# Kernel optimization log

Measured on AMD Instinct MI355X. Metric: run time of the kernel, lower is better.

## Reference

```python
import jax, jax.numpy as jnp
import numpy as np

TEMPERATURE = 0.5
W_WITHIN = 1.0
W_CROSS = 0.5
MARGIN = 0.1


def setup_inputs() -> dict:
    key = jax.random.key(0)
    k1, k2 = jax.random.split(key)
    features = jax.random.normal(k1, (8192, 256), dtype=jnp.float32)
    gene_labels = jax.random.randint(k2, (8192,), 0, 200, dtype=jnp.int64 if jax.config.jax_enable_x64 else jnp.int32)
    return {"features": features, "gene_labels": gene_labels}


def reference(features, gene_labels):
    B = features.shape[0]
    # L2-normalize rows, full pairwise cosine similarity / temperature
    fn = features / jnp.linalg.norm(features, axis=1, keepdims=True)
    sim = (fn @ fn.T) / TEMPERATURE  # [B, B]

    same = gene_labels[:, None] == gene_labels[None, :]  # [B, B]
    eye = jnp.eye(B, dtype=bool)
    same_off = same & ~eye            # same-gene, off-diagonal (gene_similarity)
    neg = ~same                       # different-gene pairs (cross_gene_mask)
    has_neg = neg.any(axis=1)

    # Per-anchor logsumexp over negatives (sim of anchor i to all different-gene samples)
    neg_sim = jnp.where(neg, sim, -jnp.inf)
    lse_neg = jax.scipy.special.logsumexp(neg_sim, axis=1)
    lse_neg = jnp.where(has_neg, lse_neg, 0.0)  # rows with no negatives are masked out below

    # Within-gene loss: for each unordered same-gene pair (i<j) with gene != -1 and
    # anchor i having >=1 negative: CE([sim_ij, neg_sims_i], label=0)
    #   = -sim_ij + logaddexp(sim_ij, lse_neg_i) = softplus(lse_neg_i - sim_ij)
    upper = jnp.triu(jnp.ones((B, B), dtype=bool), k=1)
    valid_gene = (gene_labels != -1)[:, None]
    pair_mask = same_off & upper & valid_gene & has_neg[:, None]
    within_gene_loss = jnp.where(pair_mask, jax.nn.softplus(lse_neg[:, None] - sim), 0.0).sum()

    # Cross-gene loss: mean over all ordered different-gene pairs of relu(sim - margin)
    cross_cnt = neg.sum()
    cross_sum = jnp.where(neg, jax.nn.relu(sim - MARGIN), 0.0).sum()
    cross_gene_loss = jnp.where(cross_cnt > 0, cross_sum / jnp.maximum(cross_cnt, 1).astype(sim.dtype), 0.0)

    total_loss = W_WITHIN * within_gene_loss + W_CROSS * cross_gene_loss
    num_within_gene_pairs = same_off.sum().astype(sim.dtype)
    num_cross_gene_pairs = cross_cnt
    return total_loss, within_gene_loss, cross_gene_loss, num_within_gene_pairs, num_cross_gene_pairs
```

## Files before the change

kernel.cpp:

```cpp
#include <hip/hip_runtime.h>
#include <math.h>

#define B_N   8192
#define D_K   256
#define NGENE 200
#define MAXN  512

typedef short  bf16x8 __attribute__((ext_vector_type(8)));
typedef float  f32x4  __attribute__((ext_vector_type(4)));

#define OFF_FNBF    0u
#define OFF_LPART   4194304u
#define OFF_HIST    4718592u
#define OFF_OFFS    4719616u
#define OFF_SORTED  4720640u
#define OFF_CROSSP  4753408u
#define OFF_WITHINP 4755456u
#define OFF_CCORR   4756480u

__device__ __forceinline__ unsigned short f2bf(float f) {
    unsigned int u = __float_as_uint(f);
    unsigned int r = u + 0x7fffu + ((u >> 16) & 1u);
    return (unsigned short)(r >> 16);
}
__device__ __forceinline__ float bf2f_lo(unsigned int u) { return __uint_as_float(u << 16); }
__device__ __forceinline__ float bf2f_hi(unsigned int u) { return __uint_as_float(u & 0xffff0000u); }

__global__ __launch_bounds__(256) void k_np(const float* __restrict__ feat,
                                            const int* __restrict__ lab,
                                            unsigned short* __restrict__ fnbf,
                                            int* __restrict__ hist,
                                            int* __restrict__ offs,
                                            int* __restrict__ sorted) {
    if (blockIdx.x < 2048) {
        int wave = threadIdx.x >> 6, lane = threadIdx.x & 63;
        int row  = blockIdx.x * 4 + wave;
        const float4* src = reinterpret_cast<const float4*>(feat + (size_t)row * D_K);
        float4 v = src[lane];
        float ss = v.x * v.x + v.y * v.y + v.z * v.z + v.w * v.w;
#pragma unroll
        for (int m = 1; m < 64; m <<= 1) ss += __shfl_xor(ss, m);
        float rn = 1.0f / sqrtf(ss);
        ushort4 o;
        o.x = f2bf(v.x * rn); o.y = f2bf(v.y * rn);
        o.z = f2bf(v.z * rn); o.w = f2bf(v.w * rn);
        reinterpret_cast<ushort4*>(fnbf + (size_t)row * D_K)[lane] = o;
        return;
    }
    __shared__ int sh_hist[256], sh_scan[256], sh_cur[256];
    int t = threadIdx.x;
    sh_hist[t] = 0;
    __syncthreads();
    for (int i = t; i < B_N; i += 256) {
        int lb = lab[i];
        if (lb >= 0 && lb < NGENE) atomicAdd(&sh_hist[lb], 1);
    }
    __syncthreads();
    int v = sh_hist[t];
    sh_scan[t] = v;
    __syncthreads();
#pragma unroll
    for (int d = 1; d < 256; d <<= 1) {
        int x = (t >= d) ? sh_scan[t - d] : 0;
        __syncthreads();
        sh_scan[t] += x;
        __syncthreads();
    }
    int excl = sh_scan[t] - v;
    sh_cur[t] = excl;
    if (t < NGENE) { hist[t] = v; offs[t] = excl; }
    __syncthreads();
    for (int i = t; i < B_N; i += 256) {
        int lb = lab[i];
        if (lb >= 0 && lb < NGENE) {
            int pos = atomicAdd(&sh_cur[lb], 1);
            sorted[pos] = i;
        }
    }
}

#define GLOAD8(arr, vo) do {                                                                   \
    asm volatile("global_load_dwordx4 %0, %1, %2 offset:0"   : "=v"(arr[0]) : "v"(vo), "s"(fb)); \
    asm volatile("global_load_dwordx4 %0, %1, %2 offset:64"  : "=v"(arr[1]) : "v"(vo), "s"(fb)); \
    asm volatile("global_load_dwordx4 %0, %1, %2 offset:128" : "=v"(arr[2]) : "v"(vo), "s"(fb)); \
    asm volatile("global_load_dwordx4 %0, %1, %2 offset:192" : "=v"(arr[3]) : "v"(vo), "s"(fb)); \
    asm volatile("global_load_dwordx4 %0, %1, %2 offset:256" : "=v"(arr[4]) : "v"(vo), "s"(fb)); \
    asm volatile("global_load_dwordx4 %0, %1, %2 offset:320" : "=v"(arr[5]) : "v"(vo), "s"(fb)); \
    asm volatile("global_load_dwordx4 %0, %1, %2 offset:384" : "=v"(arr[6]) : "v"(vo), "s"(fb)); \
    asm volatile("global_load_dwordx4 %0, %1, %2 offset:448" : "=v"(arr[7]) : "v"(vo), "s"(fb)); \
} while (0)

#define GL_LDS16(gp, lp)                                                          \
    __builtin_amdgcn_global_load_lds(                                             \
        (const __attribute__((address_space(1))) unsigned int*)(gp),              \
        (__attribute__((address_space(3))) unsigned int*)(lp), 16, 0, 0)

#define Z4 ((f32x4){0.f, 0.f, 0.f, 0.f})
#define MFMA(A, B, C) __builtin_amdgcn_mfma_f32_16x16x32_bf16(A, B, C, 0, 0, 0)

#define EPI(AC, LS, CS) do {                                    \
    _Pragma("unroll")                                           \
    for (int r = 0; r < 4; ++r) {                               \
        float av = AC[r];                                       \
        LS[r] += __expf(2.0f * av);                             \
        CS += fmaxf(av - 0.05f, 0.f);                           \
    }                                                           \
} while (0)

#define WAIT_VM(n) do { asm volatile("s_waitcnt vmcnt(" #n ")" ::: "memory"); \
                        __builtin_amdgcn_sched_barrier(0); } while (0)

#define WAIT_LGKM0 do { asm volatile("s_waitcnt lgkmcnt(0)" ::: "memory"); \
                        __builtin_amdgcn_sched_barrier(0); } while (0)

#define STAGE_W(BOFF, T) do {                                                      \
    const char* gt = gw + (unsigned)(T) * 8192u;                                   \
    _Pragma("unroll")                                                              \
    for (int q = 0; q < 8; ++q)                                                    \
        GL_LDS16(gt + sv[q], smem_c + wbase + (BOFF) + q * 1024u);                 \
} while (0)

__global__ __launch_bounds__(256, 2) void k_pairwise(const unsigned short* __restrict__ fnbf,
                                                     float* __restrict__ l_part,
                                                     float* __restrict__ cross_part) {
    __shared__ __align__(16) char smem_c[65536];
    __shared__ float shc[4];

    int tid = threadIdx.x;
    int wave = tid >> 6, lane = tid & 63;
    int g16 = lane >> 4, l16 = lane & 15;
    int l7 = l16 & 7;
    int rg = blockIdx.x, cwin = blockIdx.y;
    int r0 = rg * 256 + wave * 64;
    const unsigned short* fb = fnbf;
    unsigned wbase = (unsigned)wave * 16384u;

    bf16x8 a0[8], a1[8], a2[8], a3[8];
    unsigned voa = (unsigned)(r0 + l16) * 512u + (unsigned)g16 * 16u;
    GLOAD8(a0, voa); voa += 8192u;
    GLOAD8(a1, voa); voa += 8192u;
    GLOAD8(a2, voa); voa += 8192u;
    GLOAD8(a3, voa);

    const char* gw = (const char*)fnbf + (size_t)cwin * 262144u;
    unsigned sv[8];
#pragma unroll
    for (int q = 0; q < 8; ++q) {
        int f = q * 64 + lane;
        int col = f >> 5;
        sv[q] = (unsigned)(col * 512 + (((lane & 31) ^ (col & 7)) << 4));
    }

    STAGE_W(0u, 0);
    STAGE_W(8192u, 1);
    WAIT_VM(16);

    float lsum[4][4] = {};
    float cs0 = 0.f, cs1 = 0.f, cs2 = 0.f, cs3 = 0.f;
    int vb = l16 * 512;

#pragma unroll 1
    for (int st = 0; st < 32; ++st) {
        if (st < 31) { WAIT_VM(8); }
        else         { WAIT_VM(0); }

        const char* base = smem_c + wbase + (unsigned)((st & 1) << 13);
        f32x4 acc0 = Z4, acc1 = Z4, acc2 = Z4, acc3 = Z4;
#pragma unroll
        for (int ks = 0; ks < 8; ++ks) {
            const char* p = base + (unsigned)(vb + ((((ks << 2) | g16) ^ l7) << 4));
            bf16x8 bv = *(const bf16x8*)p;
            acc0 = MFMA(a0[ks], bv, acc0);
            acc1 = MFMA(a1[ks], bv, acc1);
            acc2 = MFMA(a2[ks], bv, acc2);
            acc3 = MFMA(a3[ks], bv, acc3);
        }
        EPI(acc0, lsum[0], cs0); EPI(acc1, lsum[1], cs1);
        EPI(acc2, lsum[2], cs2); EPI(acc3, lsum[3], cs3);

        if (st < 30) {
            WAIT_LGKM0;
            STAGE_W((unsigned)((st & 1) << 13), st + 2);
        }
    }

#pragma unroll
    for (int t = 0; t < 4; ++t)
#pragma unroll
        for (int r = 0; r < 4; ++r) {
            float v = lsum[t][r];
            v += __shfl_xor(v, 1); v += __shfl_xor(v, 2);
            v += __shfl_xor(v, 4); v += __shfl_xor(v, 8);
            if (l16 == 0)
                l_part[(size_t)cwin * B_N + r0 + t * 16 + g16 * 4 + r] = v;
        }

    float c = (cs0 + cs1) + (cs2 + cs3);
#pragma unroll
    for (int m = 1; m < 64; m <<= 1) c += __shfl_xor(c, m);
    if (lane == 0) shc[wave] = c;
    __syncthreads();
    if (tid == 0)
        cross_part[cwin * 32 + rg] = shc[0] + shc[1] + shc[2] + shc[3];
}

__device__ __forceinline__ float dot_g(const uint4* __restrict__ fu, int i, int j) {
    const uint4* pa = fu + (size_t)i * 32;
    const uint4* pb = fu + (size_t)j * 32;
    float d = 0.f;
#pragma unroll
    for (int k = 0; k < 32; ++k) {
        uint4 ua = pa[k], ub = pb[k];
        d = fmaf(bf2f_lo(ua.x), bf2f_lo(ub.x), d);
        d = fmaf(bf2f_hi(ua.x), bf2f_hi(ub.x), d);
        d = fmaf(bf2f_lo(ua.y), bf2f_lo(ub.y), d);
        d = fmaf(bf2f_hi(ua.y), bf2f_hi(ub.y), d);
        d = fmaf(bf2f_lo(ua.z), bf2f_lo(ub.z), d);
        d = fmaf(bf2f_hi(ua.z), bf2f_hi(ub.z), d);
        d = fmaf(bf2f_lo(ua.w), bf2f_lo(ub.w), d);
        d = fmaf(bf2f_hi(ua.w), bf2f_hi(ub.w), d);
    }
    return d;
}

__global__ __launch_bounds__(256) void k_within(const unsigned short* __restrict__ fnbf,
                                                const int* __restrict__ hist,
                                                const int* __restrict__ offs,
                                                const int* __restrict__ sorted,
                                                const float* __restrict__ l_part,
                                                float* __restrict__ within_part,
                                                float* __restrict__ cross_corr) {
    int g = blockIdx.x;
    int n = hist[g], start = offs[g];
    int t = threadIdx.x;
    int wave = t >> 6, lane = t & 63;
    int g16 = lane >> 4, l16 = lane & 15;

    __shared__ float sim[128 * 130];
    __shared__ int   rid[MAXN];
    __shared__ float slse[MAXN];
    __shared__ float red[256];

    for (int idx = t; idx < n; idx += 256) rid[idx] = sorted[start + idx];
    __syncthreads();

    float ccor = 0.f, wsum = 0.f;

    if (n <= 128) {
        int NT = (n + 15) >> 4;
        const bf16x8* fv = reinterpret_cast<const bf16x8*>(fnbf);
        for (int tile = wave; tile < NT * NT; tile += 4) {
            int ti = tile / NT, tj = tile - ti * NT;
            int ia = ti * 16 + l16;
            int ib = tj * 16 + l16;
            int ra = rid[ia < n ? ia : (n - 1)];
            int rb = rid[ib < n ? ib : (n - 1)];
            f32x4 acc = Z4;
#pragma unroll
            for (int ks = 0; ks < 8; ++ks) {
                bf16x8 av = fv[(size_t)ra * 32 + ks * 4 + g16];
                bf16x8 bv = fv[(size_t)rb * 32 + ks * 4 + g16];
                acc = MFMA(av, bv, acc);
            }
            int si = ti * 16 + g16 * 4;
            int sj = tj * 16 + l16;
#pragma unroll
            for (int r = 0; r < 4; ++r)
                sim[(si + r) * 130 + sj] = acc[r];
        }
        __syncthreads();

        for (int i = t; i < n; i += 256) {
            float raw = 0.f;
#pragma unroll
            for (int k = 0; k < 16; ++k) raw += l_part[(size_t)k * B_N + rid[i]];
            const float* srow = &sim[i * 130];
            float esum = 0.f;
            for (int j = 0; j < n; ++j) {
                float s = 2.0f * srow[j];
                esum += __expf(s);
                ccor += fmaxf(s - 0.1f, 0.f);
            }
            slse[i] = __logf(raw - esum);
        }
        __syncthreads();

        int nn = n * n;
        for (int p = t; p < nn; p += 256) {
            int i = p / n, j = p - i * n;
            if (j <= i) continue;
            float s = 2.0f * sim[i * 130 + j];
            int ai = (rid[i] < rid[j]) ? i : j;
            float x = slse[ai] - s;
            wsum += fmaxf(x, 0.f) + log1pf(__expf(-fabsf(x)));
        }
    } else {
        const uint4* fu = reinterpret_cast<const uint4*>(fnbf);
        for (int i = t; i < n; i += 256) {
            float raw = 0.f;
#pragma unroll
            for (int k = 0; k < 16; ++k) raw += l_part[(size_t)k * B_N + rid[i]];
            float esum = 0.f;
            for (int j = 0; j < n; ++j) {
                float s = 2.0f * dot_g(fu, rid[i], rid[j]);
                esum += __expf(s);
                ccor += fmaxf(s - 0.1f, 0.f);
            }
            slse[i] = __logf(raw - esum);
        }
        __syncthreads();
        int nn = n * n;
        for (int p = t; p < nn; p += 256) {
            int i = p / n, j = p - i * n;
            if (j <= i) continue;
            float s = 2.0f * dot_g(fu, rid[i], rid[j]);
            int ai = (rid[i] < rid[j]) ? i : j;
            float x = slse[ai] - s;
            wsum += fmaxf(x, 0.f) + log1pf(__expf(-fabsf(x)));
        }
    }

    red[t] = wsum;
    __syncthreads();
#pragma unroll
    for (int d2 = 128; d2 > 0; d2 >>= 1) {
        if (t < d2) red[t] += red[t + d2];
        __syncthreads();
    }
    if (t == 0) within_part[g] = red[0];
    __syncthreads();
    red[t] = ccor;
    __syncthreads();
#pragma unroll
    for (int d2 = 128; d2 > 0; d2 >>= 1) {
        if (t < d2) red[t] += red[t + d2];
        __syncthreads();
    }
    if (t == 0) cross_corr[g] = red[0];
}

__global__ __launch_bounds__(256) void k_finalize(const float* __restrict__ cross_part,
                                                  const float* __restrict__ within_part,
                                                  const float* __restrict__ cross_corr,
                                                  const int* __restrict__ hist,
                                                  float* __restrict__ out) {
    __shared__ float shc[256];
    __shared__ float shw[256];
    __shared__ float shk[256];
    __shared__ long long shs[256];
    int t = threadIdx.x;
    float cs = 0.f;
    for (int i = t; i < 512; i += 256) cs += cross_part[i];
    float wv = 0.f, cc = 0.f;
    long long s2 = 0;
    if (t < NGENE) {
        wv = within_part[t];
        cc = cross_corr[t];
        long long h = hist[t];
        s2 = h * h;
    }
    shc[t] = cs; shw[t] = wv; shk[t] = cc; shs[t] = s2;
    __syncthreads();
#pragma unroll
    for (int d = 128; d > 0; d >>= 1) {
        if (t < d) {
            shc[t] += shc[t + d]; shw[t] += shw[t + d];
            shk[t] += shk[t + d]; shs[t] += shs[t + d];
        }
        __syncthreads();
    }
    if (t == 0) {
        long long S  = shs[0];
        long long nw = S - (long long)B_N;
        long long nc = (long long)B_N * (long long)B_N - S;
        float cross_total = 2.0f * shc[0] - shk[0];
        float cross_loss = (nc > 0) ? (cross_total / (float)(nc > 1 ? nc : 1)) : 0.f;
        float within     = shw[0];
        out[0] = within + 0.5f * cross_loss;
        out[1] = within;
        out[2] = cross_loss;
        out[3] = (float)nw;
        out[4] = (float)nc;
    }
}

extern "C" void kernel_launch(void* const* d_in, const int* in_sizes, int n_in,
                              void* d_out, int out_size, void* d_ws, size_t ws_size,
                              hipStream_t stream) {
    const float* feat = (const float*)d_in[0];
    const int*   lab  = (const int*)d_in[1];
    float* out = (float*)d_out;
    char* ws = (char*)d_ws;

    unsigned short* fnbf = (unsigned short*)(ws + OFF_FNBF);
    float* l_part        = (float*)(ws + OFF_LPART);
    int*   hist          = (int*)(ws + OFF_HIST);
    int*   offs          = (int*)(ws + OFF_OFFS);
    int*   sorted        = (int*)(ws + OFF_SORTED);
    float* cross_part    = (float*)(ws + OFF_CROSSP);
    float* within_part   = (float*)(ws + OFF_WITHINP);
    float* cross_corr    = (float*)(ws + OFF_CCORR);

    k_np<<<2049, 256, 0, stream>>>(feat, lab, fnbf, hist, offs, sorted);
    k_pairwise<<<dim3(32, 16), 256, 0, stream>>>(fnbf, l_part, cross_part);
    k_within<<<NGENE, 256, 0, stream>>>(fnbf, hist, offs, sorted, l_part, within_part, cross_corr);
    k_finalize<<<1, 256, 0, stream>>>(cross_part, within_part, cross_corr, hist, out);
}
```

Baseline: 94.43 us.

## Split normalize/histogram and parallelize label bucketing across per-gene blocks

The single serial histogram, scan and scatter block inside the normalize kernel is removed. The histogram is now built with global atomics during normalization, and a new per-gene kernel scatters indices in stable order using a block-wide prefix scan. The aim is to drop the long single-block tail that serialized 8192 label loads and LDS atomics. In exchange it adds a memset and an extra kernel launch, and each of the 200 blocks rescans all labels.

```diff
diff --git a/kernel.cpp b/kernel.cpp
--- a/kernel.cpp
+++ b/kernel.cpp
@@ -26,57 +26,63 @@
 __device__ __forceinline__ float bf2f_lo(unsigned int u) { return __uint_as_float(u << 16); }
 __device__ __forceinline__ float bf2f_hi(unsigned int u) { return __uint_as_float(u & 0xffff0000u); }
 
-__global__ __launch_bounds__(256) void k_np(const float* __restrict__ feat,
-                                            const int* __restrict__ lab,
-                                            unsigned short* __restrict__ fnbf,
-                                            int* __restrict__ hist,
-                                            int* __restrict__ offs,
-                                            int* __restrict__ sorted) {
-    if (blockIdx.x < 2048) {
-        int wave = threadIdx.x >> 6, lane = threadIdx.x & 63;
-        int row  = blockIdx.x * 4 + wave;
-        const float4* src = reinterpret_cast<const float4*>(feat + (size_t)row * D_K);
-        float4 v = src[lane];
-        float ss = v.x * v.x + v.y * v.y + v.z * v.z + v.w * v.w;
-#pragma unroll
-        for (int m = 1; m < 64; m <<= 1) ss += __shfl_xor(ss, m);
-        float rn = 1.0f / sqrtf(ss);
-        ushort4 o;
-        o.x = f2bf(v.x * rn); o.y = f2bf(v.y * rn);
-        o.z = f2bf(v.z * rn); o.w = f2bf(v.w * rn);
-        reinterpret_cast<ushort4*>(fnbf + (size_t)row * D_K)[lane] = o;
-        return;
-    }
-    __shared__ int sh_hist[256], sh_scan[256], sh_cur[256];
-    int t = threadIdx.x;
-    sh_hist[t] = 0;
-    __syncthreads();
-    for (int i = t; i < B_N; i += 256) {
-        int lb = lab[i];
-        if (lb >= 0 && lb < NGENE) atomicAdd(&sh_hist[lb], 1);
-    }
-    __syncthreads();
-    int v = sh_hist[t];
-    sh_scan[t] = v;
+__global__ __launch_bounds__(256) void k_norm(const float* __restrict__ feat,
+                                              const int* __restrict__ lab,
+                                              unsigned short* __restrict__ fnbf,
+                                              int* __restrict__ hist) {
+    int wave = threadIdx.x >> 6, lane = threadIdx.x & 63;
+    int row  = blockIdx.x * 4 + wave;
+    const float4* src = reinterpret_cast<const float4*>(feat + (size_t)row * D_K);
+    float4 v = src[lane];
+    float ss = v.x * v.x + v.y * v.y + v.z * v.z + v.w * v.w;
+#pragma unroll
+    for (int m = 1; m < 64; m <<= 1) ss += __shfl_xor(ss, m);
+    float rn = 1.0f / sqrtf(ss);
+    ushort4 o;
+    o.x = f2bf(v.x * rn); o.y = f2bf(v.y * rn);
+    o.z = f2bf(v.z * rn); o.w = f2bf(v.w * rn);
+    reinterpret_cast<ushort4*>(fnbf + (size_t)row * D_K)[lane] = o;
+    if (lane == 0) {
+        int lb = lab[row];
+        if (lb >= 0 && lb < NGENE) atomicAdd(&hist[lb], 1);
+    }
+}
+
+__global__ __launch_bounds__(256) void k_scatter(const int* __restrict__ lab,
+                                                 const int* __restrict__ hist,
+                                                 int* __restrict__ offs,
+                                                 int* __restrict__ sorted) {
+    int g = blockIdx.x, t = threadIdx.x;
+    __shared__ int sc[256];
+
+    int hv = (t < NGENE) ? hist[t] : 0;
+    sc[t] = hv;
     __syncthreads();
 #pragma unroll
     for (int d = 1; d < 256; d <<= 1) {
-        int x = (t >= d) ? sh_scan[t - d] : 0;
-        __syncthreads();
-        sh_scan[t] += x;
-        __syncthreads();
-    }
-    int excl = sh_scan[t] - v;
-    sh_cur[t] = excl;
-    if (t < NGENE) { hist[t] = v; offs[t] = excl; }
-    __syncthreads();
-    for (int i = t; i < B_N; i += 256) {
-        int lb = lab[i];
-        if (lb >= 0 && lb < NGENE) {
-            int pos = atomicAdd(&sh_cur[lb], 1);
-            sorted[pos] = i;
-        }
-    }
+        int x = (t >= d) ? sc[t - d] : 0;
+        __syncthreads();
+        sc[t] += x;
+        __syncthreads();
+    }
+    int start = (g == 0) ? 0 : sc[g - 1];
+    if (t == 0) offs[g] = start;
+    __syncthreads();
+
+    int r0 = t * 32, cnt = 0;
+    for (int r = r0; r < r0 + 32; ++r) cnt += (lab[r] == g) ? 1 : 0;
+    sc[t] = cnt;
+    __syncthreads();
+#pragma unroll
+    for (int d = 1; d < 256; d <<= 1) {
+        int x = (t >= d) ? sc[t - d] : 0;
+        __syncthreads();
+        sc[t] += x;
+        __syncthreads();
+    }
+    int w = start + sc[t] - cnt;
+    for (int r = r0; r < r0 + 32; ++r)
+        if (lab[r] == g) sorted[w++] = r;
 }
 
 #define GLOAD8(arr, vo) do {                                                                   \
@@ -401,7 +407,9 @@
     float* within_part   = (float*)(ws + OFF_WITHINP);
     float* cross_corr    = (float*)(ws + OFF_CCORR);
 
-    k_np<<<2049, 256, 0, stream>>>(feat, lab, fnbf, hist, offs, sorted);
+    hipMemsetAsync(hist, 0, NGENE * sizeof(int), stream);
+    k_norm<<<B_N / 4, 256, 0, stream>>>(feat, lab, fnbf, hist);
+    k_scatter<<<NGENE, 256, 0, stream>>>(lab, hist, offs, sorted);
     k_pairwise<<<dim3(32, 16), 256, 0, stream>>>(fnbf, l_part, cross_part);
     k_within<<<NGENE, 256, 0, stream>>>(fnbf, hist, offs, sorted, l_part, within_part, cross_corr);
     k_finalize<<<1, 256, 0, stream>>>(cross_part, within_part, cross_corr, hist, out);
```

Measured after the change: 99.23 us. 5.1% more time.
